# Kernel tuning notes

Hardware: AMD Instinct MI355X
Metric: run time of the kernel (lower is better)

Reference implementation:

```python
import jax, jax.numpy as jnp
import numpy as np
import math

DIM = 2048
NUM_HEADS = 16
NUM_KV_HEADS = 4
HEAD_DIM = DIM // NUM_HEADS  # 128
KV_DIM = DIM * NUM_KV_HEADS // NUM_HEADS  # 512
B, T = 4, 2048


def setup_inputs() -> dict:
    key = jax.random.key(0)
    ks = jax.random.split(key, 12)
    s = 0.02
    return {
        "x": jax.random.normal(ks[0], (B, T, DIM), dtype=jnp.float32),
        "cos": jax.random.uniform(ks[1], (T, HEAD_DIM // 2), dtype=jnp.float32),
        "sin": jax.random.uniform(ks[2], (T, HEAD_DIM // 2), dtype=jnp.float32),
        "Wq": jax.random.normal(ks[3], (DIM, DIM), dtype=jnp.float32) * s,
        "bq": jnp.zeros((DIM,), dtype=jnp.float32),
        "Wk": jax.random.normal(ks[4], (DIM, KV_DIM), dtype=jnp.float32) * s,
        "bk": jnp.zeros((KV_DIM,), dtype=jnp.float32),
        "Wv": jax.random.normal(ks[5], (DIM, KV_DIM), dtype=jnp.float32) * s,
        "bv": jnp.zeros((KV_DIM,), dtype=jnp.float32),
        "Wo": jax.random.normal(ks[6], (DIM, DIM), dtype=jnp.float32) * s,
        "bo": jnp.zeros((DIM,), dtype=jnp.float32),
    }


def _rope(t, cos, sin):
    # t: [B, H, T, D]; cos/sin: [T, D/2] broadcast over (B, H)
    t1, t2 = t[..., ::2], t[..., 1::2]
    return jnp.concatenate([t1 * cos - t2 * sin, t1 * sin + t2 * cos], axis=-1)


def reference(x, cos, sin, Wq, bq, Wk, bk, Wv, bv, Wo, bo):
    Bx, Tx, C = x.shape
    q = (x @ Wq + bq).reshape(Bx, Tx, NUM_HEADS, HEAD_DIM).transpose(0, 2, 1, 3)
    k = (x @ Wk + bk).reshape(Bx, Tx, NUM_KV_HEADS, HEAD_DIM).transpose(0, 2, 1, 3)
    v = (x @ Wv + bv).reshape(Bx, Tx, NUM_KV_HEADS, HEAD_DIM).transpose(0, 2, 1, 3)
    rep = NUM_HEADS // NUM_KV_HEADS
    k = jnp.repeat(k, rep, axis=1)
    v = jnp.repeat(v, rep, axis=1)
    q = _rope(q, cos, sin)
    k = _rope(k, cos, sin)
    scores = jnp.einsum("bhqd,bhkd->bhqk", q, k) / math.sqrt(HEAD_DIM)
    attn = jax.nn.softmax(scores, axis=-1)
    out = jnp.einsum("bhqk,bhkd->bhqd", attn, v)
    out = out.transpose(0, 2, 1, 3).reshape(Bx, Tx, C)
    return out @ Wo + bo
```

## Files before the change

### kernel.cpp

```cpp
#include <hip/hip_runtime.h>

typedef unsigned short u16;
using bf16x8 = __attribute__((ext_vector_type(8))) short;
using u16x8  = __attribute__((ext_vector_type(8))) unsigned short;
using f32x4  = __attribute__((ext_vector_type(4))) float;
using u32x2  = __attribute__((ext_vector_type(2))) unsigned int;

__device__ __forceinline__ u16 f2bf(float f) {
  unsigned u = __float_as_uint(f);
  u += 0x7FFFu + ((u >> 16) & 1u);
  return (u16)(u >> 16);
}

__device__ __forceinline__ unsigned cvt_pk_bf16(float lo, float hi) {
  unsigned r;
  asm("v_cvt_pk_bf16_f32 %0, %1, %2" : "=v"(r) : "v"(lo), "v"(hi));
  return r;
}

__device__ __forceinline__ void gload_lds16(const void* g, void* l) {
  __builtin_amdgcn_global_load_lds(
      (const __attribute__((address_space(1))) unsigned int*)g,
      (__attribute__((address_space(3))) unsigned int*)l, 16, 0, 0);
}

__global__ __launch_bounds__(256) void k_cvt(const float* __restrict__ src,
                                             u16* __restrict__ dst) {
  size_t i = (size_t)blockIdx.x * 256 + threadIdx.x;
  const float4* s4 = (const float4*)src;
  float4 a = s4[i * 2], b = s4[i * 2 + 1];
  u16x8 r;
  r[0] = f2bf(a.x); r[1] = f2bf(a.y); r[2] = f2bf(a.z); r[3] = f2bf(a.w);
  r[4] = f2bf(b.x); r[5] = f2bf(b.y); r[6] = f2bf(b.z); r[7] = f2bf(b.w);
  *(u16x8*)(dst + i * 8) = r;
}

__global__ void k_transpose_cvt(const float* __restrict__ src, u16* __restrict__ dst,
                                int R, int C) {
  __shared__ float tile[32][33];
  int bx = blockIdx.x * 32, by = blockIdx.y * 32;
  int tx = threadIdx.x, ty = threadIdx.y;
#pragma unroll
  for (int j = 0; j < 4; ++j)
    tile[ty + j * 8][tx] = src[(size_t)(by + ty + j * 8) * C + bx + tx];
  __syncthreads();
#pragma unroll
  for (int j = 0; j < 4; ++j)
    dst[(size_t)(bx + ty + j * 8) * R + by + tx] = f2bf(tile[tx][ty + j * 8]);
}

__device__ __forceinline__ void gemm_core128(const u16* __restrict__ A,
                                             const u16* __restrict__ Bt, int K,
                                             int m0, int n0, u16* As, u16* Bs,
                                             f32x4 acc[4][4]) {
  const int tid  = threadIdx.x;
  const int lane = tid & 63;
  const int w    = tid >> 6;
  const int wr   = (w >> 1) * 64;
  const int wc   = (w & 1) * 64;
  const int srow = (w << 3) + (lane >> 3);
  const int lm   = lane & 15;
  const int lg   = lane >> 4;

  for (int kt = 0; kt < K; kt += 64) {
#pragma unroll
    for (int i = 0; i < 4; ++i) {
      int r  = (i << 5) + srow;
      int cc = (lane & 7) ^ (r & 7);
      gload_lds16(A  + (size_t)(m0 + r) * K + kt + (cc << 3), As + ((i * 4 + w) << 9));
      gload_lds16(Bt + (size_t)(n0 + r) * K + kt + (cc << 3), Bs + ((i * 4 + w) << 9));
    }
    __syncthreads();
#pragma unroll
    for (int kk = 0; kk < 2; ++kk) {
      bf16x8 af[4], bfr[4];
#pragma unroll
      for (int m = 0; m < 4; ++m) {
        const int row = wr + m * 16 + lm;
        af[m] = *(const bf16x8*)(As + row * 64 + ((((kk << 2) + lg) ^ (row & 7)) << 3));
      }
#pragma unroll
      for (int n = 0; n < 4; ++n) {
        const int row = wc + n * 16 + lm;
        bfr[n] = *(const bf16x8*)(Bs + row * 64 + ((((kk << 2) + lg) ^ (row & 7)) << 3));
      }
#pragma unroll
      for (int m = 0; m < 4; ++m)
#pragma unroll
        for (int n = 0; n < 4; ++n)
          acc[m][n] = __builtin_amdgcn_mfma_f32_16x16x32_bf16(af[m], bfr[n], acc[m][n], 0, 0, 0);
    }
    __syncthreads();
  }
}

__global__ __launch_bounds__(256, 2) void k_qkv(
    const u16* __restrict__ xb, const u16* __restrict__ wT,
    const float* __restrict__ bq, const float* __restrict__ bk, const float* __restrict__ bv,
    const float* __restrict__ cosb, const float* __restrict__ sinb,
    u16* __restrict__ qbuf, u16* __restrict__ kbuf, u16* __restrict__ vbufT) {
  __shared__ u16 As[128 * 64], Bs[128 * 64];
  const int mt = blockIdx.x, nt = blockIdx.y;
  f32x4 acc[4][4];
#pragma unroll
  for (int m = 0; m < 4; ++m)
#pragma unroll
    for (int n = 0; n < 4; ++n) { f32x4 z = {0.f, 0.f, 0.f, 0.f}; acc[m][n] = z; }
  gemm_core128(xb, wT, 2048, mt * 128, nt * 128, As, Bs, acc);

  const int lane = threadIdx.x & 63, w = threadIdx.x >> 6;
  const int row0 = mt * 128 + (w >> 1) * 64 + ((lane >> 4) << 2);
  const int col0 = nt * 128 + (w & 1) * 64 + (lane & 15);
  const float qscale = 0.12751744f;

#pragma unroll
  for (int m = 0; m < 4; ++m) {
#pragma unroll
    for (int n = 0; n < 4; ++n) {
      const int gc = col0 + n * 16;
#pragma unroll
      for (int i = 0; i < 4; ++i) {
        const int gr = row0 + m * 16 + i;
        const int b = gr >> 11, t = gr & 2047;
        float v = acc[m][n][i];
        if (nt < 16) {
          int h = gc >> 7, d = gc & 127;
          float val = v + bq[gc];
          float part = __shfl_xor(val, 1);
          int ir = d >> 1;
          float c = cosb[t * 64 + ir], s = sinb[t * 64 + ir];
          float outv; int dd;
          if (d & 1) { outv = part * s + val * c; dd = ir + 64; }
          else       { outv = val * c - part * s; dd = ir; }
          qbuf[(((size_t)(b * 16 + h) * 2048 + t) << 7) + dd] = f2bf(outv * qscale);
        } else if (nt < 20) {
          int g2 = gc - 2048;
          int kvh = g2 >> 7, d = g2 & 127;
          float val = v + bk[g2];
          float part = __shfl_xor(val, 1);
          int ir = d >> 1;
          float c = cosb[t * 64 + ir], s = sinb[t * 64 + ir];
          float outv; int dd;
          if (d & 1) { outv = part * s + val * c; dd = ir + 64; }
          else       { outv = val * c - part * s; dd = ir; }
          kbuf[(((size_t)(b * 4 + kvh) * 2048 + t) << 7) + dd] = f2bf(outv);
        } else {
          int g2 = gc - 2560;
          int kvh = g2 >> 7, d = g2 & 127;
          float val = v + bv[g2];
          vbufT[((size_t)((b * 4 + kvh) * 128 + d)) * 2048 + t] = f2bf(val);
        }
      }
    }
  }
}

__global__ __launch_bounds__(256, 2) void k_attn(const u16* __restrict__ qbuf,
                                                 const u16* __restrict__ kbuf,
                                                 const u16* __restrict__ vbufT,
                                                 u16* __restrict__ ob) {
  __shared__ u16 Ks[2][64 * 128];
  __shared__ u16 Vs[2][128 * 64];
  __shared__ u16 Ps[128 * 64];

  const int f = blockIdx.x;
  const int x = f & 7, mm = f >> 3;
  const int g = x * 2 + (mm >> 5);
  const int mem = mm & 31;
  const int b = g >> 2, kvh = g & 3;
  const int h = kvh * 4 + (mem >> 3);
  const int qt = mem & 7;

  const int tid = threadIdx.x, lane = tid & 63, w = tid >> 6;
  const int lm = lane & 15, lg = lane >> 4;

  const u16* qb = qbuf + ((size_t)((b * 16 + h) * 2048 + qt * 256)) * 128;
  const u16* kb = kbuf + ((size_t)(b * 4 + kvh) * 2048) * 128;
  const u16* vb = vbufT + ((size_t)(b * 4 + kvh) * 128) * 2048;

  bf16x8 qf[4][4];
#pragma unroll
  for (int st = 0; st < 4; ++st)
#pragma unroll
    for (int dc = 0; dc < 4; ++dc)
      qf[st][dc] = *(const bf16x8*)(qb + (size_t)(w * 64 + st * 16 + lm) * 128 + dc * 32 + (lg << 3));

  f32x4 o[4][8];
#pragma unroll
  for (int st = 0; st < 4; ++st)
#pragma unroll
    for (int dn = 0; dn < 8; ++dn) { f32x4 z = {0.f, 0.f, 0.f, 0.f}; o[st][dn] = z; }
  float lsum[4] = {0.f, 0.f, 0.f, 0.f};

  auto stage = [&](int buf, int kt) {
#pragma unroll
    for (int j = 0; j < 4; ++j) {
      int s  = w * 4 + j;
      int cK = s * 64 + lane;
      int rK = cK >> 4, ccK = cK & 15;
      gload_lds16(kb + (size_t)(kt + rK) * 128 + ((ccK ^ (rK & 7)) << 3), &Ks[buf][s << 9]);
      int dV = s * 8 + (lane >> 3), ccV = lane & 7;
      gload_lds16(vb + (size_t)dV * 2048 + kt + ((ccV ^ (dV & 7)) << 3), &Vs[buf][s << 9]);
    }
  };

  stage(0, 0);
  int cur = 0;
  for (int t = 0; t < 32; ++t) {
    const int kt = t << 6;
    if (t < 31) {
      stage(cur ^ 1, kt + 64);
      asm volatile("s_waitcnt vmcnt(8)" ::: "memory");
    } else {
      asm volatile("s_waitcnt vmcnt(0)" ::: "memory");
    }
    __builtin_amdgcn_s_barrier();
    __builtin_amdgcn_sched_barrier(0);
    const u16* KsC = Ks[cur];
    const u16* VsC = Vs[cur];

#pragma unroll
    for (int half = 0; half < 2; ++half) {
#pragma unroll
      for (int kg = 0; kg < 4; ++kg) {
        const int krow = kg * 16 + lm;
        bf16x8 kf[4];
#pragma unroll
        for (int dc = 0; dc < 4; ++dc)
          kf[dc] = *(const bf16x8*)(KsC + krow * 128 + (((dc * 4 + lg) ^ (krow & 7)) << 3));
        f32x4 s0 = {0.f, 0.f, 0.f, 0.f}, s1 = {0.f, 0.f, 0.f, 0.f};
        __builtin_amdgcn_s_setprio(1);
#pragma unroll
        for (int dc = 0; dc < 4; ++dc) {
          s0 = __builtin_amdgcn_mfma_f32_16x16x32_bf16(kf[dc], qf[half * 2 + 0][dc], s0, 0, 0, 0);
          s1 = __builtin_amdgcn_mfma_f32_16x16x32_bf16(kf[dc], qf[half * 2 + 1][dc], s1, 0, 0, 0);
        }
        __builtin_amdgcn_s_setprio(0);
#pragma unroll
        for (int st2 = 0; st2 < 2; ++st2) {
          f32x4 sv = st2 ? s1 : s0;
          float p0 = __builtin_amdgcn_exp2f(sv[0]);
          float p1 = __builtin_amdgcn_exp2f(sv[1]);
          float p2 = __builtin_amdgcn_exp2f(sv[2]);
          float p3 = __builtin_amdgcn_exp2f(sv[3]);
          lsum[half * 2 + st2] += (p0 + p1) + (p2 + p3);
          u32x2 pk;
          pk[0] = cvt_pk_bf16(p0, p1);
          pk[1] = cvt_pk_bf16(p2, p3);
          const int q = w * 32 + st2 * 16 + lm;
          const int chunk = kg * 2 + (lg >> 1);
          u16* dst = Ps + q * 64 + ((chunk ^ (q & 7)) << 3) + ((lg & 1) << 2);
          *reinterpret_cast<u32x2*>(dst) = pk;
        }
      }

#pragma unroll
      for (int kstep = 0; kstep < 2; ++kstep) {
        bf16x8 pf[2];
#pragma unroll
        for (int st2 = 0; st2 < 2; ++st2) {
          const int q = w * 32 + st2 * 16 + lm;
          pf[st2] = *(const bf16x8*)(Ps + q * 64 + (((kstep * 4 + lg) ^ (q & 7)) << 3));
        }
        __builtin_amdgcn_s_setprio(1);
#pragma unroll
        for (int dn = 0; dn < 8; ++dn) {
          const int d = dn * 16 + lm;
          bf16x8 vf = *(const bf16x8*)(VsC + d * 64 + (((kstep * 4 + lg) ^ (d & 7)) << 3));
          o[half * 2 + 0][dn] = __builtin_amdgcn_mfma_f32_16x16x32_bf16(pf[0], vf, o[half * 2 + 0][dn], 0, 0, 0);
          o[half * 2 + 1][dn] = __builtin_amdgcn_mfma_f32_16x16x32_bf16(pf[1], vf, o[half * 2 + 1][dn], 0, 0, 0);
        }
        __builtin_amdgcn_s_setprio(0);
      }
    }
    __builtin_amdgcn_sched_barrier(0);
    __builtin_amdgcn_s_barrier();
    cur ^= 1;
  }

#pragma unroll
  for (int st = 0; st < 4; ++st) {
    float L = lsum[st];
    L += __shfl_xor(L, 16);
    L += __shfl_xor(L, 32);
#pragma unroll
    for (int i = 0; i < 4; ++i) {
      float inv = 1.0f / __shfl(L, lg * 4 + i);
      int t = qt * 256 + w * 64 + st * 16 + lg * 4 + i;
#pragma unroll
      for (int dn = 0; dn < 8; ++dn) {
        int d = dn * 16 + lm;
        ob[((size_t)(b * 2048 + t)) * 2048 + h * 128 + d] = f2bf(o[st][dn][i] * inv);
      }
    }
  }
}

__global__ __launch_bounds__(256, 2) void k_oproj(const u16* __restrict__ ab,
                                                  const u16* __restrict__ woT,
                                                  const float* __restrict__ bo,
                                                  float* __restrict__ out) {
  __shared__ u16 As[128 * 64], Bs[128 * 64];
  const int mt = blockIdx.x, nt = blockIdx.y;
  f32x4 acc[4][4];
#pragma unroll
  for (int m = 0; m < 4; ++m)
#pragma unroll
    for (int n = 0; n < 4; ++n) { f32x4 z = {0.f, 0.f, 0.f, 0.f}; acc[m][n] = z; }
  gemm_core128(ab, woT, 2048, mt * 128, nt * 128, As, Bs, acc);

  const int lane = threadIdx.x & 63, w = threadIdx.x >> 6;
  const int row0 = mt * 128 + (w >> 1) * 64 + ((lane >> 4) << 2);
  const int col0 = nt * 128 + (w & 1) * 64 + (lane & 15);
#pragma unroll
  for (int m = 0; m < 4; ++m)
#pragma unroll
    for (int n = 0; n < 4; ++n) {
      const int gc = col0 + n * 16;
      const float bias = bo[gc];
#pragma unroll
      for (int i = 0; i < 4; ++i) {
        const int gr = row0 + m * 16 + i;
        out[(size_t)gr * 2048 + gc] = acc[m][n][i] + bias;
      }
    }
}

extern "C" void kernel_launch(void* const* d_in, const int* in_sizes, int n_in,
                              void* d_out, int out_size, void* d_ws, size_t ws_size,
                              hipStream_t stream) {
  const float* x    = (const float*)d_in[0];
  const float* cosb = (const float*)d_in[1];
  const float* sinb = (const float*)d_in[2];
  const float* Wq   = (const float*)d_in[3];
  const float* bq   = (const float*)d_in[4];
  const float* Wk   = (const float*)d_in[5];
  const float* bk   = (const float*)d_in[6];
  const float* Wv   = (const float*)d_in[7];
  const float* bv   = (const float*)d_in[8];
  const float* Wo   = (const float*)d_in[9];
  const float* bo   = (const float*)d_in[10];
  float* out = (float*)d_out;

  u16* ws    = (u16*)d_ws;
  u16* xb    = ws;
  u16* wqkvT = xb    + (size_t)8192 * 2048;
  u16* woT   = wqkvT + (size_t)3072 * 2048;
  u16* qbuf  = woT   + (size_t)2048 * 2048;
  u16* kbuf  = qbuf  + (size_t)8192 * 2048;
  u16* vbufT = kbuf  + (size_t)8192 * 512;
  u16* attn  = xb;

  k_cvt<<<8192, 256, 0, stream>>>(x, xb);
  dim3 tb(32, 8);
  k_transpose_cvt<<<dim3(64, 64), tb, 0, stream>>>(Wq, wqkvT, 2048, 2048);
  k_transpose_cvt<<<dim3(16, 64), tb, 0, stream>>>(Wk, wqkvT + (size_t)2048 * 2048, 2048, 512);
  k_transpose_cvt<<<dim3(16, 64), tb, 0, stream>>>(Wv, wqkvT + (size_t)2560 * 2048, 2048, 512);
  k_transpose_cvt<<<dim3(64, 64), tb, 0, stream>>>(Wo, woT, 2048, 2048);

  k_qkv<<<dim3(64, 24), 256, 0, stream>>>(xb, wqkvT, bq, bk, bv, cosb, sinb, qbuf, kbuf, vbufT);
  k_attn<<<512, 256, 0, stream>>>(qbuf, kbuf, vbufT, attn);
  k_oproj<<<dim3(64, 16), 256, 0, stream>>>(attn, woT, bo, out);
}
```

Before: 362.4 us.

## Single-buffer V, stage V during QK compute, process all 64 query rows at once

```diff
diff --git a/kernel.cpp b/kernel.cpp
--- a/kernel.cpp
+++ b/kernel.cpp
@@ -160,8 +160,8 @@
                                                  const u16* __restrict__ vbufT,
                                                  u16* __restrict__ ob) {
   __shared__ u16 Ks[2][64 * 128];
-  __shared__ u16 Vs[2][128 * 64];
-  __shared__ u16 Ps[128 * 64];
+  __shared__ u16 Vs[128 * 64];
+  __shared__ u16 Ps[256 * 64];
 
   const int f = blockIdx.x;
   const int x = f & 7, mm = f >> 3;
@@ -192,90 +192,95 @@
     for (int dn = 0; dn < 8; ++dn) { f32x4 z = {0.f, 0.f, 0.f, 0.f}; o[st][dn] = z; }
   float lsum[4] = {0.f, 0.f, 0.f, 0.f};
 
-  auto stage = [&](int buf, int kt) {
+  auto stageK = [&](int buf, int kt) {
 #pragma unroll
     for (int j = 0; j < 4; ++j) {
       int s  = w * 4 + j;
       int cK = s * 64 + lane;
       int rK = cK >> 4, ccK = cK & 15;
       gload_lds16(kb + (size_t)(kt + rK) * 128 + ((ccK ^ (rK & 7)) << 3), &Ks[buf][s << 9]);
+    }
+  };
+  auto stageV = [&](int kt) {
+#pragma unroll
+    for (int j = 0; j < 4; ++j) {
+      int s  = w * 4 + j;
       int dV = s * 8 + (lane >> 3), ccV = lane & 7;
-      gload_lds16(vb + (size_t)dV * 2048 + kt + ((ccV ^ (dV & 7)) << 3), &Vs[buf][s << 9]);
+      gload_lds16(vb + (size_t)dV * 2048 + kt + ((ccV ^ (dV & 7)) << 3), &Vs[s << 9]);
     }
   };
 
-  stage(0, 0);
-  int cur = 0;
+  stageK(0, 0);
   for (int t = 0; t < 32; ++t) {
     const int kt = t << 6;
-    if (t < 31) {
-      stage(cur ^ 1, kt + 64);
-      asm volatile("s_waitcnt vmcnt(8)" ::: "memory");
-    } else {
-      asm volatile("s_waitcnt vmcnt(0)" ::: "memory");
-    }
+    if (t < 31) stageK((t + 1) & 1, kt + 64);
+    stageV(kt);
+    if (t < 31) { asm volatile("s_waitcnt vmcnt(8)" ::: "memory"); }
+    else        { asm volatile("s_waitcnt vmcnt(4)" ::: "memory"); }
     __builtin_amdgcn_s_barrier();
     __builtin_amdgcn_sched_barrier(0);
-    const u16* KsC = Ks[cur];
-    const u16* VsC = Vs[cur];
-
-#pragma unroll
-    for (int half = 0; half < 2; ++half) {
-#pragma unroll
-      for (int kg = 0; kg < 4; ++kg) {
-        const int krow = kg * 16 + lm;
-        bf16x8 kf[4];
-#pragma unroll
-        for (int dc = 0; dc < 4; ++dc)
-          kf[dc] = *(const bf16x8*)(KsC + krow * 128 + (((dc * 4 + lg) ^ (krow & 7)) << 3));
-        f32x4 s0 = {0.f, 0.f, 0.f, 0.f}, s1 = {0.f, 0.f, 0.f, 0.f};
-        __builtin_amdgcn_s_setprio(1);
-#pragma unroll
-        for (int dc = 0; dc < 4; ++dc) {
-          s0 = __builtin_amdgcn_mfma_f32_16x16x32_bf16(kf[dc], qf[half * 2 + 0][dc], s0, 0, 0, 0);
-          s1 = __builtin_amdgcn_mfma_f32_16x16x32_bf16(kf[dc], qf[half * 2 + 1][dc], s1, 0, 0, 0);
-        }
-        __builtin_amdgcn_s_setprio(0);
-#pragma unroll
-        for (int st2 = 0; st2 < 2; ++st2) {
-          f32x4 sv = st2 ? s1 : s0;
-          float p0 = __builtin_amdgcn_exp2f(sv[0]);
-          float p1 = __builtin_amdgcn_exp2f(sv[1]);
-          float p2 = __builtin_amdgcn_exp2f(sv[2]);
-          float p3 = __builtin_amdgcn_exp2f(sv[3]);
-          lsum[half * 2 + st2] += (p0 + p1) + (p2 + p3);
-          u32x2 pk;
-          pk[0] = cvt_pk_bf16(p0, p1);
-          pk[1] = cvt_pk_bf16(p2, p3);
-          const int q = w * 32 + st2 * 16 + lm;
-          const int chunk = kg * 2 + (lg >> 1);
-          u16* dst = Ps + q * 64 + ((chunk ^ (q & 7)) << 3) + ((lg & 1) << 2);
-          *reinterpret_cast<u32x2*>(dst) = pk;
-        }
-      }
-
-#pragma unroll
-      for (int kstep = 0; kstep < 2; ++kstep) {
-        bf16x8 pf[2];
-#pragma unroll
-        for (int st2 = 0; st2 < 2; ++st2) {
-          const int q = w * 32 + st2 * 16 + lm;
-          pf[st2] = *(const bf16x8*)(Ps + q * 64 + (((kstep * 4 + lg) ^ (q & 7)) << 3));
-        }
-        __builtin_amdgcn_s_setprio(1);
-#pragma unroll
-        for (int dn = 0; dn < 8; ++dn) {
-          const int d = dn * 16 + lm;
-          bf16x8 vf = *(const bf16x8*)(VsC + d * 64 + (((kstep * 4 + lg) ^ (d & 7)) << 3));
-          o[half * 2 + 0][dn] = __builtin_amdgcn_mfma_f32_16x16x32_bf16(pf[0], vf, o[half * 2 + 0][dn], 0, 0, 0);
-          o[half * 2 + 1][dn] = __builtin_amdgcn_mfma_f32_16x16x32_bf16(pf[1], vf, o[half * 2 + 1][dn], 0, 0, 0);
-        }
-        __builtin_amdgcn_s_setprio(0);
-      }
+    const u16* KsC = Ks[t & 1];
+
+#pragma unroll
+    for (int kg = 0; kg < 4; ++kg) {
+      const int krow = kg * 16 + lm;
+      bf16x8 kf[4];
+#pragma unroll
+      for (int dc = 0; dc < 4; ++dc)
+        kf[dc] = *(const bf16x8*)(KsC + krow * 128 + (((dc * 4 + lg) ^ (krow & 7)) << 3));
+      f32x4 s[4];
+#pragma unroll
+      for (int st = 0; st < 4; ++st) { f32x4 z = {0.f, 0.f, 0.f, 0.f}; s[st] = z; }
+      __builtin_amdgcn_s_setprio(1);
+#pragma unroll
+      for (int dc = 0; dc < 4; ++dc)
+#pragma unroll
+        for (int st = 0; st < 4; ++st)
+          s[st] = __builtin_amdgcn_mfma_f32_16x16x32_bf16(kf[dc], qf[st][dc], s[st], 0, 0, 0);
+      __builtin_amdgcn_s_setprio(0);
+#pragma unroll
+      for (int st = 0; st < 4; ++st) {
+        float p0 = __builtin_amdgcn_exp2f(s[st][0]);
+        float p1 = __builtin_amdgcn_exp2f(s[st][1]);
+        float p2 = __builtin_amdgcn_exp2f(s[st][2]);
+        float p3 = __builtin_amdgcn_exp2f(s[st][3]);
+        lsum[st] += (p0 + p1) + (p2 + p3);
+        u32x2 pk;
+        pk[0] = cvt_pk_bf16(p0, p1);
+        pk[1] = cvt_pk_bf16(p2, p3);
+        const int q = w * 64 + st * 16 + lm;
+        const int chunk = kg * 2 + (lg >> 1);
+        u16* dst = Ps + q * 64 + ((chunk ^ (lm & 7)) << 3) + ((lg & 1) << 2);
+        *reinterpret_cast<u32x2*>(dst) = pk;
+      }
+    }
+
+    if (t < 31) { asm volatile("s_waitcnt vmcnt(4)" ::: "memory"); }
+    else        { asm volatile("s_waitcnt vmcnt(0)" ::: "memory"); }
+    __builtin_amdgcn_s_barrier();
+    __builtin_amdgcn_sched_barrier(0);
+
+#pragma unroll
+    for (int kstep = 0; kstep < 2; ++kstep) {
+      bf16x8 pf[4];
+#pragma unroll
+      for (int st = 0; st < 4; ++st) {
+        const int q = w * 64 + st * 16 + lm;
+        pf[st] = *(const bf16x8*)(Ps + q * 64 + (((kstep * 4 + lg) ^ (lm & 7)) << 3));
+      }
+      __builtin_amdgcn_s_setprio(1);
+#pragma unroll
+      for (int dn = 0; dn < 8; ++dn) {
+        const int d = dn * 16 + lm;
+        bf16x8 vf = *(const bf16x8*)(Vs + d * 64 + (((kstep * 4 + lg) ^ (lm & 7)) << 3));
+#pragma unroll
+        for (int st = 0; st < 4; ++st)
+          o[st][dn] = __builtin_amdgcn_mfma_f32_16x16x32_bf16(pf[st], vf, o[st][dn], 0, 0, 0);
+      }
+      __builtin_amdgcn_s_setprio(0);
     }
     __builtin_amdgcn_sched_barrier(0);
     __builtin_amdgcn_s_barrier();
-    cur ^= 1;
   }
 
 #pragma unroll
```

Result: no change. 364.6 us (+0.6%).
